# Kernel optimization log

Measured on AMD Instinct MI355X. Metric: run time of the kernel, lower is better.

The kernel has to match this reference:

```python
import jax, jax.numpy as jnp
import numpy as np

EPS_POOL = 1e-9
NEG_INF = -1e9
TEMPERATURE = 0.07


def _l2norm(x, axis=-1, eps=1e-12):
    # matches torch F.normalize(p=2): x / max(||x||, eps)
    n = jnp.sqrt(jnp.sum(x * x, axis=axis, keepdims=True))
    return x / jnp.maximum(n, eps)


def setup_inputs() -> dict:
    key = jax.random.key(0)
    ks = jax.random.split(key, 8)
    B, Lq, Lc, D = 256, 128, 512, 384
    question_tokens = jax.random.normal(ks[0], (B, Lq, D), dtype=jnp.float32)
    chunk_tokens = jax.random.normal(ks[1], (B, Lc, D), dtype=jnp.float32)
    q_mask = jax.random.randint(ks[2], (B, Lq), 0, 2, dtype=jnp.int32)
    c_mask = jax.random.randint(ks[3], (B, Lc), 0, 2, dtype=jnp.int32)
    # ensure at least one valid token per row (avoid fully-masked rows)
    q_mask = q_mask.at[:, 0].set(1)
    c_mask = c_mask.at[:, 0].set(1)
    W1 = jax.random.normal(ks[4], (D, D), dtype=jnp.float32) * (1.0 / np.sqrt(D))
    b1 = jnp.zeros((D,), dtype=jnp.float32)
    W2 = jax.random.normal(ks[5], (D, D), dtype=jnp.float32) * (1.0 / np.sqrt(D))
    b2 = jnp.zeros((D,), dtype=jnp.float32)
    return {"question_tokens": question_tokens, "chunk_tokens": chunk_tokens,
            "q_mask": q_mask, "c_mask": c_mask,
            "W1": W1, "b1": b1, "W2": W2, "b2": b2}


def _encode(tokens, mask, W1, b1, W2, b2):
    # mean pool over valid tokens: [B,L,D] -> [B,D]
    m = mask.astype(tokens.dtype)[..., None]
    pooled = jnp.sum(tokens * m, axis=1) / jnp.maximum(jnp.sum(m, axis=1), EPS_POOL)
    h = jax.nn.relu(pooled @ W1 + b1)
    proj = h @ W2 + b2
    return _l2norm(proj, axis=1)


def _late_interaction(q_tokens, c_tokens, q_mask, c_mask):
    qn = _l2norm(q_tokens)                      # [B,Lq,D]
    cn = _l2norm(c_tokens)                      # [B,Lc,D]
    sims = jnp.einsum('bqd,bkd->bqk', qn, cn)   # [B,Lq,Lc]
    valid = q_mask[:, :, None].astype(bool) & c_mask[:, None, :].astype(bool)
    sims = jnp.where(valid, sims, NEG_INF)
    max_sim = jnp.max(sims, axis=-1)            # [B,Lq]
    max_sim = jnp.where(q_mask.astype(bool), max_sim, 0.0)
    return jnp.sum(max_sim, axis=-1)            # [B]


def reference(question_tokens, chunk_tokens, q_mask, c_mask, W1, b1, W2, b2):
    q_emb = _encode(question_tokens, q_mask, W1, b1, W2, b2)  # [B,D]
    c_emb = _encode(chunk_tokens, c_mask, W1, b1, W2, b2)     # [B,D]
    contrastive_sim = (q_emb @ c_emb.T) / TEMPERATURE         # [B,B]
    late_sim = _late_interaction(question_tokens, chunk_tokens, q_mask, c_mask)  # [B]
    return contrastive_sim, late_sim
```

## Files before the change

### kernel.cpp

```cpp
#include <hip/hip_runtime.h>
#include <hip/hip_bf16.h>
#include <stdint.h>

#define NB 256
#define LQ 128
#define LC 512
#define DIM 384
#define CBP 392
#define NST 20

typedef __attribute__((ext_vector_type(8))) short short8;
typedef __attribute__((ext_vector_type(4))) float f4;
typedef __attribute__((ext_vector_type(2))) unsigned int u32x2;

__device__ __forceinline__ unsigned int pk2bf(float a, float b) {
  union { float f; uint32_t u; } x, y; x.f = a; y.f = b;
  uint32_t lo = (x.u + 0x7fffu + ((x.u >> 16) & 1u)) >> 16;
  uint32_t hi = (y.u + 0x7fffu + ((y.u >> 16) & 1u)) >> 16;
  return lo | (hi << 16);
}

__global__ __launch_bounds__(512, 2)
void fused2(const float* __restrict__ qtok, const float* __restrict__ ctok,
            const int* __restrict__ qm, const int* __restrict__ cm,
            float* __restrict__ pooled, float* __restrict__ late) {
  __shared__ unsigned short s_cb[2][32][CBP];
  __shared__ float s_qi[LQ];
  __shared__ float s_ci[2][32];
  __shared__ int s_qm[LQ];
  __shared__ int s_cm[LC];
  __shared__ float s_cnt[16];
  __shared__ float s_wsum[8];

  const int b = blockIdx.x, tid = threadIdx.x;
  const int wave = tid >> 6, lane = tid & 63;
  const int rA = lane & 15, hi = lane >> 4;
  const bool hiHalf = lane >= 32;
  const int l31 = lane & 31;

  const float* qb = qtok + (size_t)b * LQ * DIM;
  const float* cb = ctok + (size_t)b * LC * DIM;

  s_cm[tid] = cm[b * LC + tid];
  if (tid < LQ) s_qm[tid] = qm[b * LQ + tid];
  __syncthreads();

  f4 v0[4], h0[2], v1[4], h1[2];
  f4 pqA = {0,0,0,0}, pqB = {0,0,0,0}, pcA = {0,0,0,0}, pcB = {0,0,0,0};
  float cq = 0.f, cc = 0.f;
  float rm[4] = {-1e9f, -1e9f, -1e9f, -1e9f};
  short8 A[12] = {};

#define TBASE(t) (((t) < 4) ? (qb + (size_t)(t) * 32 * DIM) \
                            : (cb + (size_t)((t) - 4) * 32 * DIM))

#define ISSUE(V, H, base_) do {                                              \
    const float* bb_ = (base_);                                              \
    _Pragma("unroll")                                                        \
    for (int i_ = 0; i_ < 4; ++i_)                                           \
      V[i_] = *((const f4*)(bb_ + (size_t)(wave * 4 + i_) * DIM) + lane);    \
    _Pragma("unroll")                                                        \
    for (int j_ = 0; j_ < 2; ++j_)                                           \
      H[j_] = *((const f4*)(bb_ + (size_t)(wave * 4 + 2 * j_ +               \
                (hiHalf ? 1 : 0)) * DIM) + 64 + l31);                        \
  } while (0)

#define STAGE(T, V, H, BUF) do {                                             \
    const int t_ = (T);                                                      \
    if (t_ == NST - 1) { asm volatile("s_waitcnt vmcnt(0)" ::: "memory"); }  \
    else               { asm volatile("s_waitcnt vmcnt(6)" ::: "memory"); }  \
    __builtin_amdgcn_sched_barrier(0);                                       \
    const bool isq_ = t_ < 4;                                                \
    const int* mk_ = isq_ ? (s_qm + t_ * 32) : (s_cm + (t_ - 4) * 32);       \
    float ss_[4];                                                            \
    _Pragma("unroll")                                                        \
    for (int i_ = 0; i_ < 4; ++i_) {                                         \
      const int lr_ = wave * 4 + i_;                                         \
      u32x2 w_; w_[0] = pk2bf(V[i_].x, V[i_].y); w_[1] = pk2bf(V[i_].z, V[i_].w); \
      *(u32x2*)&s_cb[BUF][lr_][4 * lane] = w_;                               \
      ss_[i_] = V[i_].x * V[i_].x + V[i_].y * V[i_].y                        \
              + V[i_].z * V[i_].z + V[i_].w * V[i_].w;                       \
    }                                                                        \
    _Pragma("unroll")                                                        \
    for (int j_ = 0; j_ < 2; ++j_) {                                         \
      const int lr_ = wave * 4 + 2 * j_ + (hiHalf ? 1 : 0);                  \
      u32x2 w_; w_[0] = pk2bf(H[j_].x, H[j_].y); w_[1] = pk2bf(H[j_].z, H[j_].w); \
      *(u32x2*)&s_cb[BUF][lr_][256 + 4 * l31] = w_;                          \
      const float td_ = H[j_].x * H[j_].x + H[j_].y * H[j_].y               \
                      + H[j_].z * H[j_].z + H[j_].w * H[j_].w;              \
      if (hiHalf) ss_[2 * j_ + 1] += td_; else ss_[2 * j_] += td_;           \
    }                                                                        \
    _Pragma("unroll")                                                        \
    for (int o_ = 32; o_; o_ >>= 1) {                                        \
      _Pragma("unroll")                                                      \
      for (int i_ = 0; i_ < 4; ++i_) ss_[i_] += __shfl_xor(ss_[i_], o_);     \
    }                                                                        \
    float fm_[4];                                                            \
    _Pragma("unroll")                                                        \
    for (int i_ = 0; i_ < 4; ++i_) fm_[i_] = (float)mk_[wave * 4 + i_];      \
    if (isq_) {                                                              \
      _Pragma("unroll")                                                      \
      for (int i_ = 0; i_ < 4; ++i_) { pqA += V[i_] * fm_[i_]; cq += fm_[i_]; } \
      _Pragma("unroll")                                                      \
      for (int j_ = 0; j_ < 2; ++j_)                                         \
        pqB += H[j_] * (hiHalf ? fm_[2 * j_ + 1] : fm_[2 * j_]);             \
      if (lane == 0) {                                                       \
        _Pragma("unroll")                                                    \
        for (int i_ = 0; i_ < 4; ++i_)                                       \
          s_qi[t_ * 32 + wave * 4 + i_] = 1.0f / fmaxf(sqrtf(ss_[i_]), 1e-12f); \
      }                                                                      \
    } else {                                                                 \
      _Pragma("unroll")                                                      \
      for (int i_ = 0; i_ < 4; ++i_) { pcA += V[i_] * fm_[i_]; cc += fm_[i_]; } \
      _Pragma("unroll")                                                      \
      for (int j_ = 0; j_ < 2; ++j_)                                         \
        pcB += H[j_] * (hiHalf ? fm_[2 * j_ + 1] : fm_[2 * j_]);             \
      if (lane == 0) {                                                       \
        _Pragma("unroll")                                                    \
        for (int i_ = 0; i_ < 4; ++i_)                                       \
          s_ci[BUF][wave * 4 + i_] = 1.0f / fmaxf(sqrtf(ss_[i_]), 1e-12f);   \
      }                                                                      \
    }                                                                        \
    if (t_ + 2 < NST) { ISSUE(V, H, TBASE(t_ + 2)); }                        \
    asm volatile("s_waitcnt lgkmcnt(0)" ::: "memory");                       \
    __builtin_amdgcn_s_barrier();                                            \
    __builtin_amdgcn_sched_barrier(0);                                       \
    if (isq_) {                                                              \
      if ((wave >> 1) == t_) {                                               \
        const int lb_ = (wave & 1) * 16 + rA;                                \
        _Pragma("unroll")                                                    \
        for (int kk_ = 0; kk_ < 12; ++kk_)                                   \
          A[kk_] = *(const short8*)&s_cb[BUF][lb_][kk_ * 32 + hi * 8];       \
        asm volatile("s_waitcnt lgkmcnt(0)" ::: "memory");                   \
        __builtin_amdgcn_sched_barrier(0);                                   \
      }                                                                      \
    } else {                                                                 \
      f4 a0_ = {0,0,0,0}, a1_ = {0,0,0,0};                                   \
      _Pragma("unroll")                                                      \
      for (int kk_ = 0; kk_ < 12; ++kk_) {                                   \
        const short8 b0_ = *(const short8*)&s_cb[BUF][rA][kk_ * 32 + hi * 8];     \
        const short8 b1_ = *(const short8*)&s_cb[BUF][rA + 16][kk_ * 32 + hi * 8];\
        a0_ = __builtin_amdgcn_mfma_f32_16x16x32_bf16(A[kk_], b0_, a0_, 0, 0, 0); \
        a1_ = __builtin_amdgcn_mfma_f32_16x16x32_bf16(A[kk_], b1_, a1_, 0, 0, 0); \
      }                                                                      \
      const int tb_ = (t_ - 4) * 32;                                         \
      const bool m0_ = s_cm[tb_ + rA] != 0;                                  \
      const bool m1_ = s_cm[tb_ + rA + 16] != 0;                             \
      const float ci0_ = s_ci[BUF][rA], ci1_ = s_ci[BUF][rA + 16];           \
      _Pragma("unroll")                                                      \
      for (int r_ = 0; r_ < 4; ++r_) {                                       \
        const float qi_ = s_qi[wave * 16 + hi * 4 + r_];                     \
        const float x0_ = m0_ ? a0_[r_] * (qi_ * ci0_) : -1e9f;              \
        const float x1_ = m1_ ? a1_[r_] * (qi_ * ci1_) : -1e9f;              \
        rm[r_] = fmaxf(rm[r_], fmaxf(x0_, x1_));                             \
      }                                                                      \
    }                                                                        \
  } while (0)

  ISSUE(v0, h0, TBASE(0));
  ISSUE(v1, h1, TBASE(1));

  for (int t = 0; t < NST; t += 2) {
    STAGE(t, v0, h0, 0);
    STAGE(t + 1, v1, h1, 1);
  }

#pragma unroll
  for (int r = 0; r < 4; ++r) {
#pragma unroll
    for (int o = 1; o < 16; o <<= 1) rm[r] = fmaxf(rm[r], __shfl_xor(rm[r], o));
  }
  float ps = 0.f;
  if (rA == 0) {
    const int rowb = wave * 16 + hi * 4;
#pragma unroll
    for (int r = 0; r < 4; ++r) ps += s_qm[rowb + r] ? rm[r] : 0.f;
  }
#pragma unroll
  for (int o = 32; o; o >>= 1) ps += __shfl_xor(ps, o);
  if (lane == 0) s_wsum[wave] = ps;

  __syncthreads();

  float* red = (float*)&s_cb[0][0][0];
  *(f4*)&red[(wave * 2 + 0) * 512 + 4 * lane] = pqA;
  *(f4*)&red[(wave * 2 + 0) * 512 + 256 + (hiHalf ? 128 : 0) + 4 * l31] = pqB;
  *(f4*)&red[(wave * 2 + 1) * 512 + 4 * lane] = pcA;
  *(f4*)&red[(wave * 2 + 1) * 512 + 256 + (hiHalf ? 128 : 0) + 4 * l31] = pcB;
  if (lane == 0) { s_cnt[wave] = cq; s_cnt[8 + wave] = cc; }
  __syncthreads();

  if (tid < DIM) {
    float sq = 0.f, sc = 0.f, nq = 0.f, nc = 0.f;
    if (tid < 256) {
#pragma unroll
      for (int w = 0; w < 8; ++w) {
        sq += red[(w * 2 + 0) * 512 + tid];
        sc += red[(w * 2 + 1) * 512 + tid];
      }
    } else {
#pragma unroll
      for (int w = 0; w < 8; ++w) {
        sq += red[(w * 2 + 0) * 512 + tid] + red[(w * 2 + 0) * 512 + tid + 128];
        sc += red[(w * 2 + 1) * 512 + tid] + red[(w * 2 + 1) * 512 + tid + 128];
      }
    }
#pragma unroll
    for (int w = 0; w < 8; ++w) { nq += s_cnt[w]; nc += s_cnt[8 + w]; }
    pooled[b * DIM + tid] = sq / fmaxf(nq, 1e-9f);
    pooled[(NB + b) * DIM + tid] = sc / fmaxf(nc, 1e-9f);
  }
  if (tid == 0) {
    float tot = 0.f;
#pragma unroll
    for (int w = 0; w < 8; ++w) tot += s_wsum[w];
    late[b] = tot;
  }
}

__global__ __launch_bounds__(DIM)
void mlp_v1(const float* __restrict__ pooled,
            const float* __restrict__ W1, const float* __restrict__ b1,
            const float* __restrict__ W2, const float* __restrict__ b2,
            float* __restrict__ emb) {
  __shared__ float s_in[DIM];
  __shared__ float s_h[DIM];
  __shared__ float s_red[6];
  const int row = blockIdx.y * NB + blockIdx.x;
  const int d = threadIdx.x;
  s_in[d] = pooled[(size_t)row * DIM + d];
  __syncthreads();
  float acc = b1[d];
#pragma unroll 8
  for (int k = 0; k < DIM; ++k) acc = fmaf(s_in[k], W1[k * DIM + d], acc);
  s_h[d] = fmaxf(acc, 0.f);
  __syncthreads();
  float p = b2[d];
#pragma unroll 8
  for (int k = 0; k < DIM; ++k) p = fmaf(s_h[k], W2[k * DIM + d], p);
  float ss = p * p;
#pragma unroll
  for (int o = 32; o; o >>= 1) ss += __shfl_xor(ss, o);
  if ((d & 63) == 0) s_red[d >> 6] = ss;
  __syncthreads();
  float tot = 0.f;
#pragma unroll
  for (int w = 0; w < 6; ++w) tot += s_red[w];
  emb[(size_t)row * DIM + d] = p * (1.0f / fmaxf(sqrtf(tot), 1e-12f));
}

__global__ __launch_bounds__(NB)
void contrast_kernel(const float* __restrict__ emb, float* __restrict__ out0) {
  __shared__ float s_q[DIM];
  const int i = blockIdx.x;
  for (int k = threadIdx.x; k < DIM; k += NB) s_q[k] = emb[(size_t)i * DIM + k];
  __syncthreads();
  const float* ce = emb + (size_t)(NB + threadIdx.x) * DIM;
  float acc = 0.f;
#pragma unroll 8
  for (int k = 0; k < DIM; ++k) acc = fmaf(s_q[k], ce[k], acc);
  out0[(size_t)i * NB + threadIdx.x] = acc / 0.07f;
}

extern "C" void kernel_launch(void* const* d_in, const int* in_sizes, int n_in,
                              void* d_out, int out_size, void* d_ws, size_t ws_size,
                              hipStream_t stream) {
  const float* qtok = (const float*)d_in[0];
  const float* ctok = (const float*)d_in[1];
  const int*   qmm  = (const int*)d_in[2];
  const int*   cmm  = (const int*)d_in[3];
  const float* W1   = (const float*)d_in[4];
  const float* b1   = (const float*)d_in[5];
  const float* W2   = (const float*)d_in[6];
  const float* b2   = (const float*)d_in[7];

  float* out0 = (float*)d_out;
  float* late = out0 + NB * NB;
  float* pooled = (float*)d_ws;
  float* emb    = pooled + 2 * NB * DIM;

  hipLaunchKernelGGL(fused2, dim3(NB), dim3(512), 0, stream,
                     qtok, ctok, qmm, cmm, pooled, late);
  hipLaunchKernelGGL(mlp_v1, dim3(NB, 2), dim3(DIM), 0, stream,
                     pooled, W1, b1, W2, b2, emb);
  hipLaunchKernelGGL(contrast_kernel, dim3(NB), dim3(NB), 0, stream, emb, out0);
}
```

Measured before the change: 108.5 us.

## Split chunk dimension across two blocks per batch and merge in MLP kernel

The fused late-interaction/pooling kernel now launches two blocks per batch row, each handling half of the chunk tokens (12 stages instead of 20), and writes partial row-max values, partial pooled sums and counts to workspace. A new merge_mlp kernel combines the partial maxima and sums, computes the late score, and runs the q and c MLPs together in one block so the W1/W2 loads are shared. This doubles the grid on a large-CU GPU and reduces the per-block serial stage count. In exchange, every block re-reads and re-normalizes the question tokens, and extra workspace traffic is added.

```diff
diff --git a/kernel.cpp b/kernel.cpp
--- a/kernel.cpp
+++ b/kernel.cpp
@@ -7,7 +7,7 @@
 #define LC 512
 #define DIM 384
 #define CBP 392
-#define NST 20
+#define NST 12
 
 typedef __attribute__((ext_vector_type(8))) short short8;
 typedef __attribute__((ext_vector_type(4))) float f4;
@@ -21,27 +21,29 @@
 }
 
 __global__ __launch_bounds__(512, 2)
-void fused2(const float* __restrict__ qtok, const float* __restrict__ ctok,
+void fused3(const float* __restrict__ qtok, const float* __restrict__ ctok,
             const int* __restrict__ qm, const int* __restrict__ cm,
-            float* __restrict__ pooled, float* __restrict__ late) {
+            float* __restrict__ ws_rm, float* __restrict__ pp_q,
+            float* __restrict__ pp_c, float* __restrict__ nn_q,
+            float* __restrict__ nn_c) {
   __shared__ unsigned short s_cb[2][32][CBP];
   __shared__ float s_qi[LQ];
   __shared__ float s_ci[2][32];
   __shared__ int s_qm[LQ];
-  __shared__ int s_cm[LC];
+  __shared__ int s_cm[256];
   __shared__ float s_cnt[16];
-  __shared__ float s_wsum[8];
-
-  const int b = blockIdx.x, tid = threadIdx.x;
+
+  const int bid = blockIdx.x, tid = threadIdx.x;
+  const int b = bid >> 1, half = bid & 1;
   const int wave = tid >> 6, lane = tid & 63;
   const int rA = lane & 15, hi = lane >> 4;
   const bool hiHalf = lane >= 32;
   const int l31 = lane & 31;
 
   const float* qb = qtok + (size_t)b * LQ * DIM;
-  const float* cb = ctok + (size_t)b * LC * DIM;
-
-  s_cm[tid] = cm[b * LC + tid];
+  const float* cbh = ctok + (size_t)b * LC * DIM + (size_t)half * 256 * DIM;
+
+  if (tid < 256) s_cm[tid] = cm[b * LC + half * 256 + tid];
   if (tid < LQ) s_qm[tid] = qm[b * LQ + tid];
   __syncthreads();
 
@@ -52,7 +54,7 @@
   short8 A[12] = {};
 
 #define TBASE(t) (((t) < 4) ? (qb + (size_t)(t) * 32 * DIM) \
-                            : (cb + (size_t)((t) - 4) * 32 * DIM))
+                            : (cbh + (size_t)((t) - 4) * 32 * DIM))
 
 #define ISSUE(V, H, base_) do {                                              \
     const float* bb_ = (base_);                                              \
@@ -170,16 +172,11 @@
 #pragma unroll
     for (int o = 1; o < 16; o <<= 1) rm[r] = fmaxf(rm[r], __shfl_xor(rm[r], o));
   }
-  float ps = 0.f;
   if (rA == 0) {
-    const int rowb = wave * 16 + hi * 4;
-#pragma unroll
-    for (int r = 0; r < 4; ++r) ps += s_qm[rowb + r] ? rm[r] : 0.f;
-  }
-#pragma unroll
-  for (int o = 32; o; o >>= 1) ps += __shfl_xor(ps, o);
-  if (lane == 0) s_wsum[wave] = ps;
-
+#pragma unroll
+    for (int r = 0; r < 4; ++r)
+      ws_rm[(size_t)bid * LQ + wave * 16 + hi * 4 + r] = rm[r];
+  }
   __syncthreads();
 
   float* red = (float*)&s_cb[0][0][0];
@@ -207,46 +204,69 @@
     }
 #pragma unroll
     for (int w = 0; w < 8; ++w) { nq += s_cnt[w]; nc += s_cnt[8 + w]; }
-    pooled[b * DIM + tid] = sq / fmaxf(nq, 1e-9f);
-    pooled[(NB + b) * DIM + tid] = sc / fmaxf(nc, 1e-9f);
-  }
-  if (tid == 0) {
-    float tot = 0.f;
-#pragma unroll
-    for (int w = 0; w < 8; ++w) tot += s_wsum[w];
-    late[b] = tot;
+    if (half == 0) pp_q[(size_t)b * DIM + tid] = sq;
+    pp_c[(size_t)bid * DIM + tid] = sc;
+    if (tid == 0) {
+      if (half == 0) nn_q[b] = nq;
+      nn_c[bid] = nc;
+    }
   }
 }
 
 __global__ __launch_bounds__(DIM)
-void mlp_v1(const float* __restrict__ pooled,
-            const float* __restrict__ W1, const float* __restrict__ b1,
-            const float* __restrict__ W2, const float* __restrict__ b2,
-            float* __restrict__ emb) {
-  __shared__ float s_in[DIM];
-  __shared__ float s_h[DIM];
-  __shared__ float s_red[6];
-  const int row = blockIdx.y * NB + blockIdx.x;
+void merge_mlp(const float* __restrict__ ws_rm, const float* __restrict__ pp_q,
+               const float* __restrict__ pp_c, const float* __restrict__ nn_q,
+               const float* __restrict__ nn_c, const int* __restrict__ qm,
+               const float* __restrict__ W1, const float* __restrict__ b1,
+               const float* __restrict__ W2, const float* __restrict__ b2,
+               float* __restrict__ late, float* __restrict__ emb) {
+  __shared__ float s_q[DIM], s_c[DIM], s_hq[DIM], s_hc[DIM];
+  __shared__ float s_red[2][6], s_l[2];
+  const int b = blockIdx.x;
   const int d = threadIdx.x;
-  s_in[d] = pooled[(size_t)row * DIM + d];
-  __syncthreads();
-  float acc = b1[d];
+
+  if (d < LQ) {
+    const float m = fmaxf(ws_rm[(size_t)(2 * b) * LQ + d],
+                          ws_rm[(size_t)(2 * b + 1) * LQ + d]);
+    float ps = qm[b * LQ + d] ? m : 0.f;
+#pragma unroll
+    for (int o = 32; o; o >>= 1) ps += __shfl_xor(ps, o);
+    if ((d & 63) == 0) s_l[d >> 6] = ps;
+  }
+  const float nqv = fmaxf(nn_q[b], 1e-9f);
+  const float ncv = fmaxf(nn_c[2 * b] + nn_c[2 * b + 1], 1e-9f);
+  s_q[d] = pp_q[(size_t)b * DIM + d] / nqv;
+  s_c[d] = (pp_c[(size_t)(2 * b) * DIM + d] + pp_c[(size_t)(2 * b + 1) * DIM + d]) / ncv;
+  __syncthreads();
+
+  float aq = b1[d], ac = b1[d];
 #pragma unroll 8
-  for (int k = 0; k < DIM; ++k) acc = fmaf(s_in[k], W1[k * DIM + d], acc);
-  s_h[d] = fmaxf(acc, 0.f);
-  __syncthreads();
-  float p = b2[d];
+  for (int k = 0; k < DIM; ++k) {
+    const float w = W1[k * DIM + d];
+    aq = fmaf(s_q[k], w, aq);
+    ac = fmaf(s_c[k], w, ac);
+  }
+  s_hq[d] = fmaxf(aq, 0.f);
+  s_hc[d] = fmaxf(ac, 0.f);
+  __syncthreads();
+  float pq = b2[d], pc = b2[d];
 #pragma unroll 8
-  for (int k = 0; k < DIM; ++k) p = fmaf(s_h[k], W2[k * DIM + d], p);
-  float ss = p * p;
-#pragma unroll
-  for (int o = 32; o; o >>= 1) ss += __shfl_xor(ss, o);
-  if ((d & 63) == 0) s_red[d >> 6] = ss;
-  __syncthreads();
-  float tot = 0.f;
-#pragma unroll
-  for (int w = 0; w < 6; ++w) tot += s_red[w];
-  emb[(size_t)row * DIM + d] = p * (1.0f / fmaxf(sqrtf(tot), 1e-12f));
+  for (int k = 0; k < DIM; ++k) {
+    const float w = W2[k * DIM + d];
+    pq = fmaf(s_hq[k], w, pq);
+    pc = fmaf(s_hc[k], w, pc);
+  }
+  float q2 = pq * pq, c2 = pc * pc;
+#pragma unroll
+  for (int o = 32; o; o >>= 1) { q2 += __shfl_xor(q2, o); c2 += __shfl_xor(c2, o); }
+  if ((d & 63) == 0) { s_red[0][d >> 6] = q2; s_red[1][d >> 6] = c2; }
+  __syncthreads();
+  float tq = 0.f, tc = 0.f;
+#pragma unroll
+  for (int w = 0; w < 6; ++w) { tq += s_red[0][w]; tc += s_red[1][w]; }
+  emb[(size_t)b * DIM + d] = pq * (1.0f / fmaxf(sqrtf(tq), 1e-12f));
+  emb[(size_t)(NB + b) * DIM + d] = pc * (1.0f / fmaxf(sqrtf(tc), 1e-12f));
+  if (d == 0) late[b] = s_l[0] + s_l[1];
 }
 
 __global__ __launch_bounds__(NB)
@@ -276,12 +296,18 @@
 
   float* out0 = (float*)d_out;
   float* late = out0 + NB * NB;
-  float* pooled = (float*)d_ws;
-  float* emb    = pooled + 2 * NB * DIM;
-
-  hipLaunchKernelGGL(fused2, dim3(NB), dim3(512), 0, stream,
-                     qtok, ctok, qmm, cmm, pooled, late);
-  hipLaunchKernelGGL(mlp_v1, dim3(NB, 2), dim3(DIM), 0, stream,
-                     pooled, W1, b1, W2, b2, emb);
+
+  float* ws_rm = (float*)d_ws;
+  float* pp_q  = ws_rm + (size_t)2 * NB * LQ;
+  float* pp_c  = pp_q + (size_t)NB * DIM;
+  float* nn_q  = pp_c + (size_t)2 * NB * DIM;
+  float* nn_c  = nn_q + NB;
+  float* emb   = nn_c + 2 * NB;
+
+  hipLaunchKernelGGL(fused3, dim3(2 * NB), dim3(512), 0, stream,
+                     qtok, ctok, qmm, cmm, ws_rm, pp_q, pp_c, nn_q, nn_c);
+  hipLaunchKernelGGL(merge_mlp, dim3(NB), dim3(DIM), 0, stream,
+                     ws_rm, pp_q, pp_c, nn_q, nn_c, qmm, W1, b1, W2, b2,
+                     late, emb);
   hipLaunchKernelGGL(contrast_kernel, dim3(NB), dim3(NB), 0, stream, emb, out0);
 }
```

After: 121.3 us. +11.8%, slower.

## Double block to 1024 threads splitting chunk columns across wave halves

Applied to the files above, without the earlier changes.

The fused late-interaction and pooling kernel now runs with 16 waves per block instead of 8. Each wave loads half as many rows per stage, and the two wave groups each handle 16 of the 32 chunk columns in the MFMA similarity step. Partial row maxima are merged through shared memory. This roughly halves per-thread register and load work and raises the number of memory requests in flight per block. In exchange, occupancy drops to one block per CU, shared-memory use grows with a dedicated reduction buffer, and each stage barrier now synchronises twice as many waves.

```diff
diff --git a/kernel.cpp b/kernel.cpp
--- a/kernel.cpp
+++ b/kernel.cpp
@@ -20,20 +20,23 @@
   return lo | (hi << 16);
 }
 
-__global__ __launch_bounds__(512, 2)
-void fused2(const float* __restrict__ qtok, const float* __restrict__ ctok,
+__global__ __launch_bounds__(1024, 1)
+void fused4(const float* __restrict__ qtok, const float* __restrict__ ctok,
             const int* __restrict__ qm, const int* __restrict__ cm,
             float* __restrict__ pooled, float* __restrict__ late) {
   __shared__ unsigned short s_cb[2][32][CBP];
+  __shared__ float s_red[16][2][512];
   __shared__ float s_qi[LQ];
   __shared__ float s_ci[2][32];
   __shared__ int s_qm[LQ];
   __shared__ int s_cm[LC];
-  __shared__ float s_cnt[16];
-  __shared__ float s_wsum[8];
+  __shared__ float s_cnt[32];
+  __shared__ float s_rmh[2][LQ];
+  __shared__ float s_wsum[2];
 
   const int b = blockIdx.x, tid = threadIdx.x;
   const int wave = tid >> 6, lane = tid & 63;
+  const int W7 = wave & 7, CH = wave >> 3;
   const int rA = lane & 15, hi = lane >> 4;
   const bool hiHalf = lane >= 32;
   const int l31 = lane & 31;
@@ -41,11 +44,12 @@
   const float* qb = qtok + (size_t)b * LQ * DIM;
   const float* cb = ctok + (size_t)b * LC * DIM;
 
-  s_cm[tid] = cm[b * LC + tid];
+  if (tid < LC) s_cm[tid] = cm[b * LC + tid];
   if (tid < LQ) s_qm[tid] = qm[b * LQ + tid];
   __syncthreads();
 
-  f4 v0[4], h0[2], v1[4], h1[2];
+  f4 v0[2], v1[2];
+  f4 h0, h1;
   f4 pqA = {0,0,0,0}, pqB = {0,0,0,0}, pcA = {0,0,0,0}, pcB = {0,0,0,0};
   float cq = 0.f, cc = 0.f;
   float rm[4] = {-1e9f, -1e9f, -1e9f, -1e9f};
@@ -57,68 +61,57 @@
 #define ISSUE(V, H, base_) do {                                              \
     const float* bb_ = (base_);                                              \
     _Pragma("unroll")                                                        \
-    for (int i_ = 0; i_ < 4; ++i_)                                           \
-      V[i_] = *((const f4*)(bb_ + (size_t)(wave * 4 + i_) * DIM) + lane);    \
-    _Pragma("unroll")                                                        \
-    for (int j_ = 0; j_ < 2; ++j_)                                           \
-      H[j_] = *((const f4*)(bb_ + (size_t)(wave * 4 + 2 * j_ +               \
-                (hiHalf ? 1 : 0)) * DIM) + 64 + l31);                        \
+    for (int i_ = 0; i_ < 2; ++i_)                                           \
+      V[i_] = *((const f4*)(bb_ + (size_t)(wave * 2 + i_) * DIM) + lane);    \
+    H = *((const f4*)(bb_ + (size_t)(wave * 2 + (hiHalf ? 1 : 0)) * DIM)     \
+          + 64 + l31);                                                       \
   } while (0)
 
 #define STAGE(T, V, H, BUF) do {                                             \
     const int t_ = (T);                                                      \
     if (t_ == NST - 1) { asm volatile("s_waitcnt vmcnt(0)" ::: "memory"); }  \
-    else               { asm volatile("s_waitcnt vmcnt(6)" ::: "memory"); }  \
+    else               { asm volatile("s_waitcnt vmcnt(3)" ::: "memory"); }  \
     __builtin_amdgcn_sched_barrier(0);                                       \
     const bool isq_ = t_ < 4;                                                \
     const int* mk_ = isq_ ? (s_qm + t_ * 32) : (s_cm + (t_ - 4) * 32);       \
-    float ss_[4];                                                            \
+    float ss_[2];                                                            \
     _Pragma("unroll")                                                        \
-    for (int i_ = 0; i_ < 4; ++i_) {                                         \
-      const int lr_ = wave * 4 + i_;                                         \
+    for (int i_ = 0; i_ < 2; ++i_) {                                         \
+      const int lr_ = wave * 2 + i_;                                         \
       u32x2 w_; w_[0] = pk2bf(V[i_].x, V[i_].y); w_[1] = pk2bf(V[i_].z, V[i_].w); \
       *(u32x2*)&s_cb[BUF][lr_][4 * lane] = w_;                               \
       ss_[i_] = V[i_].x * V[i_].x + V[i_].y * V[i_].y                        \
               + V[i_].z * V[i_].z + V[i_].w * V[i_].w;                       \
     }                                                                        \
-    _Pragma("unroll")                                                        \
-    for (int j_ = 0; j_ < 2; ++j_) {                                         \
-      const int lr_ = wave * 4 + 2 * j_ + (hiHalf ? 1 : 0);                  \
-      u32x2 w_; w_[0] = pk2bf(H[j_].x, H[j_].y); w_[1] = pk2bf(H[j_].z, H[j_].w); \
+    {                                                                        \
+      const int lr_ = wave * 2 + (hiHalf ? 1 : 0);                           \
+      u32x2 w_; w_[0] = pk2bf(H.x, H.y); w_[1] = pk2bf(H.z, H.w);            \
       *(u32x2*)&s_cb[BUF][lr_][256 + 4 * l31] = w_;                          \
-      const float td_ = H[j_].x * H[j_].x + H[j_].y * H[j_].y               \
-                      + H[j_].z * H[j_].z + H[j_].w * H[j_].w;              \
-      if (hiHalf) ss_[2 * j_ + 1] += td_; else ss_[2 * j_] += td_;           \
+      const float td_ = H.x * H.x + H.y * H.y + H.z * H.z + H.w * H.w;       \
+      if (hiHalf) ss_[1] += td_; else ss_[0] += td_;                         \
     }                                                                        \
     _Pragma("unroll")                                                        \
     for (int o_ = 32; o_; o_ >>= 1) {                                        \
-      _Pragma("unroll")                                                      \
-      for (int i_ = 0; i_ < 4; ++i_) ss_[i_] += __shfl_xor(ss_[i_], o_);     \
-    }                                                                        \
-    float fm_[4];                                                            \
-    _Pragma("unroll")                                                        \
-    for (int i_ = 0; i_ < 4; ++i_) fm_[i_] = (float)mk_[wave * 4 + i_];      \
+      ss_[0] += __shfl_xor(ss_[0], o_);                                      \
+      ss_[1] += __shfl_xor(ss_[1], o_);                                      \
+    }                                                                        \
+    float fm_[2];                                                            \
+    fm_[0] = (float)mk_[wave * 2]; fm_[1] = (float)mk_[wave * 2 + 1];        \
     if (isq_) {                                                              \
-      _Pragma("unroll")                                                      \
-      for (int i_ = 0; i_ < 4; ++i_) { pqA += V[i_] * fm_[i_]; cq += fm_[i_]; } \
-      _Pragma("unroll")                                                      \
-      for (int j_ = 0; j_ < 2; ++j_)                                         \
-        pqB += H[j_] * (hiHalf ? fm_[2 * j_ + 1] : fm_[2 * j_]);             \
+      pqA += V[0] * fm_[0] + V[1] * fm_[1];                                  \
+      pqB += H * (hiHalf ? fm_[1] : fm_[0]);                                 \
+      cq += fm_[0] + fm_[1];                                                 \
       if (lane == 0) {                                                       \
-        _Pragma("unroll")                                                    \
-        for (int i_ = 0; i_ < 4; ++i_)                                       \
-          s_qi[t_ * 32 + wave * 4 + i_] = 1.0f / fmaxf(sqrtf(ss_[i_]), 1e-12f); \
+        s_qi[t_ * 32 + wave * 2]     = 1.0f / fmaxf(sqrtf(ss_[0]), 1e-12f);  \
+        s_qi[t_ * 32 + wave * 2 + 1] = 1.0f / fmaxf(sqrtf(ss_[1]), 1e-12f);  \
       }                                                                      \
     } else {                                                                 \
-      _Pragma("unroll")                                                      \
-      for (int i_ = 0; i_ < 4; ++i_) { pcA += V[i_] * fm_[i_]; cc += fm_[i_]; } \
-      _Pragma("unroll")                                                      \
-      for (int j_ = 0; j_ < 2; ++j_)                                         \
-        pcB += H[j_] * (hiHalf ? fm_[2 * j_ + 1] : fm_[2 * j_]);             \
+      pcA += V[0] * fm_[0] + V[1] * fm_[1];                                  \
+      pcB += H * (hiHalf ? fm_[1] : fm_[0]);                                 \
+      cc += fm_[0] + fm_[1];                                                 \
       if (lane == 0) {                                                       \
-        _Pragma("unroll")                                                    \
-        for (int i_ = 0; i_ < 4; ++i_)                                       \
-          s_ci[BUF][wave * 4 + i_] = 1.0f / fmaxf(sqrtf(ss_[i_]), 1e-12f);   \
+        s_ci[BUF][wave * 2]     = 1.0f / fmaxf(sqrtf(ss_[0]), 1e-12f);       \
+        s_ci[BUF][wave * 2 + 1] = 1.0f / fmaxf(sqrtf(ss_[1]), 1e-12f);       \
       }                                                                      \
     }                                                                        \
     if (t_ + 2 < NST) { ISSUE(V, H, TBASE(t_ + 2)); }                        \
@@ -126,8 +119,8 @@
     __builtin_amdgcn_s_barrier();                                            \
     __builtin_amdgcn_sched_barrier(0);                                       \
     if (isq_) {                                                              \
-      if ((wave >> 1) == t_) {                                               \
-        const int lb_ = (wave & 1) * 16 + rA;                                \
+      if ((W7 >> 1) == t_) {                                                 \
+        const int lb_ = (W7 & 1) * 16 + rA;                                  \
         _Pragma("unroll")                                                    \
         for (int kk_ = 0; kk_ < 12; ++kk_)                                   \
           A[kk_] = *(const short8*)&s_cb[BUF][lb_][kk_ * 32 + hi * 8];       \
@@ -135,24 +128,20 @@
         __builtin_amdgcn_sched_barrier(0);                                   \
       }                                                                      \
     } else {                                                                 \
-      f4 a0_ = {0,0,0,0}, a1_ = {0,0,0,0};                                   \
+      f4 a0_ = {0,0,0,0};                                                    \
       _Pragma("unroll")                                                      \
       for (int kk_ = 0; kk_ < 12; ++kk_) {                                   \
-        const short8 b0_ = *(const short8*)&s_cb[BUF][rA][kk_ * 32 + hi * 8];     \
-        const short8 b1_ = *(const short8*)&s_cb[BUF][rA + 16][kk_ * 32 + hi * 8];\
+        const short8 b0_ = *(const short8*)&s_cb[BUF][CH * 16 + rA][kk_ * 32 + hi * 8]; \
         a0_ = __builtin_amdgcn_mfma_f32_16x16x32_bf16(A[kk_], b0_, a0_, 0, 0, 0); \
-        a1_ = __builtin_amdgcn_mfma_f32_16x16x32_bf16(A[kk_], b1_, a1_, 0, 0, 0); \
       }                                                                      \
       const int tb_ = (t_ - 4) * 32;                                         \
-      const bool m0_ = s_cm[tb_ + rA] != 0;                                  \
-      const bool m1_ = s_cm[tb_ + rA + 16] != 0;                             \
-      const float ci0_ = s_ci[BUF][rA], ci1_ = s_ci[BUF][rA + 16];           \
+      const bool m0_ = s_cm[tb_ + CH * 16 + rA] != 0;                        \
+      const float ci0_ = s_ci[BUF][CH * 16 + rA];                            \
       _Pragma("unroll")                                                      \
       for (int r_ = 0; r_ < 4; ++r_) {                                       \
-        const float qi_ = s_qi[wave * 16 + hi * 4 + r_];                     \
+        const float qi_ = s_qi[W7 * 16 + hi * 4 + r_];                       \
         const float x0_ = m0_ ? a0_[r_] * (qi_ * ci0_) : -1e9f;              \
-        const float x1_ = m1_ ? a1_[r_] * (qi_ * ci1_) : -1e9f;              \
-        rm[r_] = fmaxf(rm[r_], fmaxf(x0_, x1_));                             \
+        rm[r_] = fmaxf(rm[r_], x0_);                                         \
       }                                                                      \
     }                                                                        \
   } while (0)
@@ -170,52 +159,49 @@
 #pragma unroll
     for (int o = 1; o < 16; o <<= 1) rm[r] = fmaxf(rm[r], __shfl_xor(rm[r], o));
   }
-  float ps = 0.f;
   if (rA == 0) {
-    const int rowb = wave * 16 + hi * 4;
-#pragma unroll
-    for (int r = 0; r < 4; ++r) ps += s_qm[rowb + r] ? rm[r] : 0.f;
-  }
-#pragma unroll
-  for (int o = 32; o; o >>= 1) ps += __shfl_xor(ps, o);
-  if (lane == 0) s_wsum[wave] = ps;
-
-  __syncthreads();
-
-  float* red = (float*)&s_cb[0][0][0];
-  *(f4*)&red[(wave * 2 + 0) * 512 + 4 * lane] = pqA;
-  *(f4*)&red[(wave * 2 + 0) * 512 + 256 + (hiHalf ? 128 : 0) + 4 * l31] = pqB;
-  *(f4*)&red[(wave * 2 + 1) * 512 + 4 * lane] = pcA;
-  *(f4*)&red[(wave * 2 + 1) * 512 + 256 + (hiHalf ? 128 : 0) + 4 * l31] = pcB;
-  if (lane == 0) { s_cnt[wave] = cq; s_cnt[8 + wave] = cc; }
+#pragma unroll
+    for (int r = 0; r < 4; ++r)
+      s_rmh[CH][W7 * 16 + hi * 4 + r] = rm[r];
+  }
+
+  *(f4*)&s_red[wave][0][4 * lane] = pqA;
+  *(f4*)&s_red[wave][0][256 + (hiHalf ? 128 : 0) + 4 * l31] = pqB;
+  *(f4*)&s_red[wave][1][4 * lane] = pcA;
+  *(f4*)&s_red[wave][1][256 + (hiHalf ? 128 : 0) + 4 * l31] = pcB;
+  if (lane == 0) { s_cnt[wave] = cq; s_cnt[16 + wave] = cc; }
   __syncthreads();
 
   if (tid < DIM) {
     float sq = 0.f, sc = 0.f, nq = 0.f, nc = 0.f;
     if (tid < 256) {
 #pragma unroll
-      for (int w = 0; w < 8; ++w) {
-        sq += red[(w * 2 + 0) * 512 + tid];
-        sc += red[(w * 2 + 1) * 512 + tid];
+      for (int w = 0; w < 16; ++w) {
+        sq += s_red[w][0][tid];
+        sc += s_red[w][1][tid];
       }
     } else {
 #pragma unroll
-      for (int w = 0; w < 8; ++w) {
-        sq += red[(w * 2 + 0) * 512 + tid] + red[(w * 2 + 0) * 512 + tid + 128];
-        sc += red[(w * 2 + 1) * 512 + tid] + red[(w * 2 + 1) * 512 + tid + 128];
+      for (int w = 0; w < 16; ++w) {
+        sq += s_red[w][0][tid] + s_red[w][0][tid + 128];
+        sc += s_red[w][1][tid] + s_red[w][1][tid + 128];
       }
     }
 #pragma unroll
-    for (int w = 0; w < 8; ++w) { nq += s_cnt[w]; nc += s_cnt[8 + w]; }
+    for (int w = 0; w < 16; ++w) { nq += s_cnt[w]; nc += s_cnt[16 + w]; }
     pooled[b * DIM + tid] = sq / fmaxf(nq, 1e-9f);
     pooled[(NB + b) * DIM + tid] = sc / fmaxf(nc, 1e-9f);
   }
-  if (tid == 0) {
-    float tot = 0.f;
-#pragma unroll
-    for (int w = 0; w < 8; ++w) tot += s_wsum[w];
-    late[b] = tot;
-  }
+
+  if (tid < LQ) {
+    const float m = fmaxf(s_rmh[0][tid], s_rmh[1][tid]);
+    float ps = s_qm[tid] ? m : 0.f;
+#pragma unroll
+    for (int o = 32; o; o >>= 1) ps += __shfl_xor(ps, o);
+    if ((tid & 63) == 0) s_wsum[tid >> 6] = ps;
+  }
+  __syncthreads();
+  if (tid == 0) late[b] = s_wsum[0] + s_wsum[1];
 }
 
 __global__ __launch_bounds__(DIM)
@@ -279,7 +265,7 @@
   float* pooled = (float*)d_ws;
   float* emb    = pooled + 2 * NB * DIM;
 
-  hipLaunchKernelGGL(fused2, dim3(NB), dim3(512), 0, stream,
+  hipLaunchKernelGGL(fused4, dim3(NB), dim3(1024), 0, stream,
                      qtok, ctok, qmm, cmm, pooled, late);
   hipLaunchKernelGGL(mlp_v1, dim3(NB, 2), dim3(DIM), 0, stream,
                      pooled, W1, b1, W2, b2, emb);
```

Result: slower. 193.2 us (+78.1%).

## Keep question tile in shared memory and deepen global-load prefetch to three stages

Applied to the files above, without the earlier changes.

The question tokens are now stored as bf16 in a dedicated LDS array, and each MFMA step reads its A fragments from LDS. Before, the A operands were held in 12 short8 registers per lane. The global prefetch pipeline goes from two to three in-flight stages, with adjusted vmcnt waits and a third register buffer set, to better hide HBM latency. The trade is fewer registers for A against more LDS traffic per MFMA and about 100KB of LDS per block, which may limit occupancy to one block per CU despite the launch bound of two.

```diff
diff --git a/kernel.cpp b/kernel.cpp
--- a/kernel.cpp
+++ b/kernel.cpp
@@ -8,6 +8,7 @@
 #define DIM 384
 #define CBP 392
 #define NST 20
+#define NQS 4
 
 typedef __attribute__((ext_vector_type(8))) short short8;
 typedef __attribute__((ext_vector_type(4))) float f4;
@@ -21,10 +22,11 @@
 }
 
 __global__ __launch_bounds__(512, 2)
-void fused2(const float* __restrict__ qtok, const float* __restrict__ ctok,
+void fused6(const float* __restrict__ qtok, const float* __restrict__ ctok,
             const int* __restrict__ qm, const int* __restrict__ cm,
             float* __restrict__ pooled, float* __restrict__ late) {
-  __shared__ unsigned short s_cb[2][32][CBP];
+  __shared__ unsigned short s_q[LQ][CBP];
+  __shared__ unsigned short s_c[2][32][CBP];
   __shared__ float s_qi[LQ];
   __shared__ float s_ci[2][32];
   __shared__ int s_qm[LQ];
@@ -45,14 +47,13 @@
   if (tid < LQ) s_qm[tid] = qm[b * LQ + tid];
   __syncthreads();
 
-  f4 v0[4], h0[2], v1[4], h1[2];
+  f4 v0[4], h0[2], v1[4], h1[2], v2[4], h2[2];
   f4 pqA = {0,0,0,0}, pqB = {0,0,0,0}, pcA = {0,0,0,0}, pcB = {0,0,0,0};
   float cq = 0.f, cc = 0.f;
   float rm[4] = {-1e9f, -1e9f, -1e9f, -1e9f};
-  short8 A[12] = {};
-
-#define TBASE(t) (((t) < 4) ? (qb + (size_t)(t) * 32 * DIM) \
-                            : (cb + (size_t)((t) - 4) * 32 * DIM))
+
+#define TBASE(t) (((t) < NQS) ? (qb + (size_t)(t) * 32 * DIM) \
+                              : (cb + (size_t)((t) - NQS) * 32 * DIM))
 
 #define ISSUE(V, H, base_) do {                                              \
     const float* bb_ = (base_);                                              \
@@ -65,19 +66,22 @@
                 (hiHalf ? 1 : 0)) * DIM) + 64 + l31);                        \
   } while (0)
 
-#define STAGE(T, V, H, BUF) do {                                             \
+#define STAGE(T, V, H) do {                                                  \
     const int t_ = (T);                                                      \
-    if (t_ == NST - 1) { asm volatile("s_waitcnt vmcnt(0)" ::: "memory"); }  \
-    else               { asm volatile("s_waitcnt vmcnt(6)" ::: "memory"); }  \
+    if      (t_ == NST - 1) { asm volatile("s_waitcnt vmcnt(0)" ::: "memory"); } \
+    else if (t_ == NST - 2) { asm volatile("s_waitcnt vmcnt(6)" ::: "memory"); } \
+    else                    { asm volatile("s_waitcnt vmcnt(12)" ::: "memory"); } \
     __builtin_amdgcn_sched_barrier(0);                                       \
-    const bool isq_ = t_ < 4;                                                \
-    const int* mk_ = isq_ ? (s_qm + t_ * 32) : (s_cm + (t_ - 4) * 32);       \
+    const bool isq_ = t_ < NQS;                                              \
+    const int cbuf_ = (t_ - NQS) & 1;                                        \
+    const int* mk_ = isq_ ? (s_qm + t_ * 32) : (s_cm + (t_ - NQS) * 32);     \
+    unsigned short* dst_ = isq_ ? &s_q[t_ * 32][0] : &s_c[cbuf_][0][0];      \
     float ss_[4];                                                            \
     _Pragma("unroll")                                                        \
     for (int i_ = 0; i_ < 4; ++i_) {                                         \
       const int lr_ = wave * 4 + i_;                                         \
       u32x2 w_; w_[0] = pk2bf(V[i_].x, V[i_].y); w_[1] = pk2bf(V[i_].z, V[i_].w); \
-      *(u32x2*)&s_cb[BUF][lr_][4 * lane] = w_;                               \
+      *(u32x2*)(dst_ + (size_t)lr_ * CBP + 4 * lane) = w_;                   \
       ss_[i_] = V[i_].x * V[i_].x + V[i_].y * V[i_].y                        \
               + V[i_].z * V[i_].z + V[i_].w * V[i_].w;                       \
     }                                                                        \
@@ -85,7 +89,7 @@
     for (int j_ = 0; j_ < 2; ++j_) {                                         \
       const int lr_ = wave * 4 + 2 * j_ + (hiHalf ? 1 : 0);                  \
       u32x2 w_; w_[0] = pk2bf(H[j_].x, H[j_].y); w_[1] = pk2bf(H[j_].z, H[j_].w); \
-      *(u32x2*)&s_cb[BUF][lr_][256 + 4 * l31] = w_;                          \
+      *(u32x2*)(dst_ + (size_t)lr_ * CBP + 256 + 4 * l31) = w_;              \
       const float td_ = H[j_].x * H[j_].x + H[j_].y * H[j_].y               \
                       + H[j_].z * H[j_].z + H[j_].w * H[j_].w;              \
       if (hiHalf) ss_[2 * j_ + 1] += td_; else ss_[2 * j_] += td_;           \
@@ -118,35 +122,27 @@
       if (lane == 0) {                                                       \
         _Pragma("unroll")                                                    \
         for (int i_ = 0; i_ < 4; ++i_)                                       \
-          s_ci[BUF][wave * 4 + i_] = 1.0f / fmaxf(sqrtf(ss_[i_]), 1e-12f);   \
-      }                                                                      \
-    }                                                                        \
-    if (t_ + 2 < NST) { ISSUE(V, H, TBASE(t_ + 2)); }                        \
+          s_ci[cbuf_][wave * 4 + i_] = 1.0f / fmaxf(sqrtf(ss_[i_]), 1e-12f); \
+      }                                                                      \
+    }                                                                        \
+    if (t_ + 3 < NST) { ISSUE(V, H, TBASE(t_ + 3)); }                        \
     asm volatile("s_waitcnt lgkmcnt(0)" ::: "memory");                       \
     __builtin_amdgcn_s_barrier();                                            \
     __builtin_amdgcn_sched_barrier(0);                                       \
-    if (isq_) {                                                              \
-      if ((wave >> 1) == t_) {                                               \
-        const int lb_ = (wave & 1) * 16 + rA;                                \
-        _Pragma("unroll")                                                    \
-        for (int kk_ = 0; kk_ < 12; ++kk_)                                   \
-          A[kk_] = *(const short8*)&s_cb[BUF][lb_][kk_ * 32 + hi * 8];       \
-        asm volatile("s_waitcnt lgkmcnt(0)" ::: "memory");                   \
-        __builtin_amdgcn_sched_barrier(0);                                   \
-      }                                                                      \
-    } else {                                                                 \
+    if (!isq_) {                                                             \
       f4 a0_ = {0,0,0,0}, a1_ = {0,0,0,0};                                   \
       _Pragma("unroll")                                                      \
       for (int kk_ = 0; kk_ < 12; ++kk_) {                                   \
-        const short8 b0_ = *(const short8*)&s_cb[BUF][rA][kk_ * 32 + hi * 8];     \
-        const short8 b1_ = *(const short8*)&s_cb[BUF][rA + 16][kk_ * 32 + hi * 8];\
-        a0_ = __builtin_amdgcn_mfma_f32_16x16x32_bf16(A[kk_], b0_, a0_, 0, 0, 0); \
-        a1_ = __builtin_amdgcn_mfma_f32_16x16x32_bf16(A[kk_], b1_, a1_, 0, 0, 0); \
-      }                                                                      \
-      const int tb_ = (t_ - 4) * 32;                                         \
+        const short8 af_ = *(const short8*)&s_q[wave * 16 + rA][kk_ * 32 + hi * 8]; \
+        const short8 b0_ = *(const short8*)&s_c[cbuf_][rA][kk_ * 32 + hi * 8];      \
+        const short8 b1_ = *(const short8*)&s_c[cbuf_][rA + 16][kk_ * 32 + hi * 8]; \
+        a0_ = __builtin_amdgcn_mfma_f32_16x16x32_bf16(af_, b0_, a0_, 0, 0, 0);      \
+        a1_ = __builtin_amdgcn_mfma_f32_16x16x32_bf16(af_, b1_, a1_, 0, 0, 0);      \
+      }                                                                      \
+      const int tb_ = (t_ - NQS) * 32;                                       \
       const bool m0_ = s_cm[tb_ + rA] != 0;                                  \
       const bool m1_ = s_cm[tb_ + rA + 16] != 0;                             \
-      const float ci0_ = s_ci[BUF][rA], ci1_ = s_ci[BUF][rA + 16];           \
+      const float ci0_ = s_ci[cbuf_][rA], ci1_ = s_ci[cbuf_][rA + 16];       \
       _Pragma("unroll")                                                      \
       for (int r_ = 0; r_ < 4; ++r_) {                                       \
         const float qi_ = s_qi[wave * 16 + hi * 4 + r_];                     \
@@ -159,11 +155,15 @@
 
   ISSUE(v0, h0, TBASE(0));
   ISSUE(v1, h1, TBASE(1));
-
-  for (int t = 0; t < NST; t += 2) {
-    STAGE(t, v0, h0, 0);
-    STAGE(t + 1, v1, h1, 1);
-  }
+  ISSUE(v2, h2, TBASE(2));
+
+  for (int t = 0; t < 18; t += 3) {
+    STAGE(t, v0, h0);
+    STAGE(t + 1, v1, h1);
+    STAGE(t + 2, v2, h2);
+  }
+  STAGE(18, v0, h0);
+  STAGE(19, v1, h1);
 
 #pragma unroll
   for (int r = 0; r < 4; ++r) {
@@ -182,7 +182,7 @@
 
   __syncthreads();
 
-  float* red = (float*)&s_cb[0][0][0];
+  float* red = (float*)&s_q[0][0];
   *(f4*)&red[(wave * 2 + 0) * 512 + 4 * lane] = pqA;
   *(f4*)&red[(wave * 2 + 0) * 512 + 256 + (hiHalf ? 128 : 0) + 4 * l31] = pqB;
   *(f4*)&red[(wave * 2 + 1) * 512 + 4 * lane] = pcA;
@@ -279,7 +279,7 @@
   float* pooled = (float*)d_ws;
   float* emb    = pooled + 2 * NB * DIM;
 
-  hipLaunchKernelGGL(fused2, dim3(NB), dim3(512), 0, stream,
+  hipLaunchKernelGGL(fused6, dim3(NB), dim3(512), 0, stream,
                      qtok, ctok, qmm, cmm, pooled, late);
   hipLaunchKernelGGL(mlp_v1, dim3(NB, 2), dim3(DIM), 0, stream,
                      pooled, W1, b1, W2, b2, emb);
```

Result: slower. 113.1 us (+4.3%).
